# Performance work log

Hardware: AMD Instinct MI355X
Metric: run time of the kernel (lower is better)

The kernel has to match this reference:

```python
import jax, jax.numpy as jnp
import numpy as np

N = 100000   # nodes
E = 1600000  # edges
D = 128      # in = hid = out feature dim
EPS = 1e-5


def gcn_conv(x, W, b, src, dst, w, n):
    # PyG GCNConv: h = x W; symmetric normalization with self-loops already in (src,dst,w)
    h = x @ W                                        # [N, D]
    deg = jax.ops.segment_sum(w, dst, num_segments=n)
    dinv = jnp.where(deg > 0, deg ** -0.5, 0.0)
    norm = dinv[src] * w * dinv[dst]                 # [E+N]
    out = jax.ops.segment_sum(h[src] * norm[:, None], dst, num_segments=n)
    return out + b


def batch_norm(x, gamma, beta):
    m = x.mean(axis=0)
    v = x.var(axis=0)  # biased, as PyTorch uses for normalization
    return gamma * (x - m) * jax.lax.rsqrt(v + EPS) + beta


def setup_inputs() -> dict:
    key = jax.random.key(0)
    ks = jax.random.split(key, 10)
    x = jax.random.normal(ks[0], (N, D), dtype=jnp.float32)
    edge_index = jax.random.randint(ks[1], (2, E), 0, N, dtype=jnp.int64)
    edge_weight = jax.random.uniform(ks[2], (E,), dtype=jnp.float32)
    s = 1.0 / np.sqrt(D)
    W1 = jax.random.uniform(ks[3], (D, D), jnp.float32, -s, s)
    b1 = jax.random.uniform(ks[4], (D,), jnp.float32, -s, s)
    W2 = jax.random.uniform(ks[5], (D, D), jnp.float32, -s, s)
    b2 = jax.random.uniform(ks[6], (D,), jnp.float32, -s, s)
    g1 = jnp.ones((D,), jnp.float32); beta1 = jnp.zeros((D,), jnp.float32)
    g2 = jnp.ones((D,), jnp.float32); beta2 = jnp.zeros((D,), jnp.float32)
    return {"x": x, "edge_index": edge_index, "edge_weight": edge_weight,
            "W1": W1, "b1": b1, "W2": W2, "b2": b2,
            "g1": g1, "beta1": beta1, "g2": g2, "beta2": beta2}


def reference(x, edge_index, edge_weight, W1, b1, W2, b2, g1, beta1, g2, beta2):
    loops = jnp.arange(N, dtype=edge_index.dtype)
    src = jnp.concatenate([edge_index[0], loops])
    dst = jnp.concatenate([edge_index[1], loops])
    w = jnp.concatenate([edge_weight, jnp.ones((N,), edge_weight.dtype)])
    # layer 1: GCNConv -> BN -> relu (dropout inactive in eval)
    h = gcn_conv(x, W1, b1, src, dst, w, N)
    h = jax.nn.relu(batch_norm(h, g1, beta1))
    # layer 2
    h = gcn_conv(h, W2, b2, src, dst, w, N)
    h = jax.nn.relu(batch_norm(h, g2, beta2))
    return h
```

## Files before the change

kernel.cpp:

```cpp
#include <hip/hip_runtime.h>
#include <hip/hip_bf16.h>

#define NN 100000
#define EE 1600000
#define DD 128
#define CAP 56
#define NB 391
#define CAPB 6144
#define NRG 6250
#define NC 16
#define BN_EPS 1e-5f

typedef __attribute__((ext_vector_type(8))) short short8;
typedef __attribute__((ext_vector_type(4))) float f32x4;
typedef __attribute__((ext_vector_type(4))) unsigned int u32x4;

__device__ __forceinline__ float bfu2f(unsigned short u) {
    return __uint_as_float(((unsigned int)u) << 16);
}
__device__ __forceinline__ unsigned short f2bfu(float f) {
    unsigned int u = __float_as_uint(f);
    unsigned int r = (u + 0x7fffu + ((u >> 16) & 1u)) >> 16;
    return (unsigned short)r;
}
__device__ __forceinline__ void atomAddF(float* p, float v) {
    unsafeAtomicAdd(p, v);
}
__device__ __forceinline__ float ldF(const void* __restrict__ p, int isf32, size_t idx) {
    return isf32 ? ((const float*)p)[idx]
                 : bfu2f(((const unsigned short*)p)[idx]);
}
__device__ __forceinline__ int edge_at(const int* __restrict__ ei, int is64, unsigned int pos) {
    return is64 ? ei[(size_t)pos * 2] : ei[pos];
}

__global__ __launch_bounds__(256) void prep2(const int* __restrict__ ei,
                                             const unsigned int* __restrict__ g1w,
                                             const void* __restrict__ W1,
                                             const void* __restrict__ W2,
                                             int* __restrict__ flags,
                                             unsigned int* __restrict__ cursor,
                                             float* __restrict__ stats,
                                             unsigned short* __restrict__ Wt1,
                                             unsigned short* __restrict__ Wt2) {
    int t = threadIdx.x;
    int b = blockIdx.x;
    int isf32 = (g1w[0] == 0x3F800000u) ? 1 : 0;
    if (b == 0) {
        __shared__ int nz;
        if (t == 0) nz = 0;
        __syncthreads();
        if (ei[2 * t + 1] != 0) atomicExch(&nz, 1);
        __syncthreads();
        if (t == 0) {
            flags[0] = (nz == 0) ? 1 : 0;
            flags[1] = isf32;
        }
        stats[t] = 0.f;
        stats[512 + t] = 0.f;
    } else if (b == 129) {
        for (int i = t; i < 512; i += 256) cursor[i] = 0;
    } else {
        int i = (b - 1) * 256 + t;
        if (i < 16384) {
            int r = i >> 7, c = i & 127;
            Wt1[c * DD + r] = f2bfu(ldF(W1, isf32, i));
        } else {
            int j = i - 16384;
            int r = j >> 7, c = j & 127;
            Wt2[c * DD + r] = f2bfu(ldF(W2, isf32, j));
        }
    }
}

__device__ __forceinline__ void load_arow(const void* __restrict__ Xv, int isf32,
                                          int row, int quad, short8* dst) {
#pragma unroll
    for (int k4 = 0; k4 < 4; ++k4) {
        int k = k4 * 32 + quad * 8;
        if (isf32) {
            const float* xf = (const float*)Xv + (size_t)row * DD + k;
            float4 f0 = *(const float4*)xf;
            float4 f1 = *(const float4*)(xf + 4);
            short8 a;
            a[0] = (short)f2bfu(f0.x); a[1] = (short)f2bfu(f0.y);
            a[2] = (short)f2bfu(f0.z); a[3] = (short)f2bfu(f0.w);
            a[4] = (short)f2bfu(f1.x); a[5] = (short)f2bfu(f1.y);
            a[6] = (short)f2bfu(f1.z); a[7] = (short)f2bfu(f1.w);
            dst[k4] = a;
        } else {
            dst[k4] = *(const short8*)((const short*)Xv + (size_t)row * DD + k);
        }
    }
}

__global__ __launch_bounds__(256) void fatk(const void* __restrict__ Xv,
                                            const int* __restrict__ flags,
                                            const unsigned short* __restrict__ Wt,
                                            unsigned short* __restrict__ H,
                                            const int* __restrict__ ei,
                                            const void* __restrict__ w,
                                            uint2* __restrict__ staging,
                                            unsigned int* __restrict__ cursor) {
    unsigned int g = blockIdx.x;
    unsigned int q = g / 3u, r = g % 3u;
    if (r == 2u) {
        __shared__ unsigned int cnt[NB], base[NB];
        for (int i = threadIdx.x; i < NB; i += 256) cnt[i] = 0;
        __syncthreads();
        int is64 = flags[0], isf32 = flags[1];
        unsigned int e0 = q * 2048u;
        unsigned int lo[8], hi[8], rk[8];
        int bk[8];
#pragma unroll
        for (int i = 0; i < 8; ++i) {
            unsigned int e = e0 + i * 256u + threadIdx.x;
            bk[i] = -1;
            if (e < EE) {
                int s = edge_at(ei, is64, e);
                int d = edge_at(ei, is64, EE + e);
                float wv = ldF(w, isf32, e);
                unsigned int wfix = __float2uint_rn(wv * 16777216.0f);
                wfix = wfix > 0xFFFFFFu ? 0xFFFFFFu : wfix;
                lo[i] = ((unsigned int)f2bfu(wv) << 17) | (unsigned int)s;
                hi[i] = (wfix << 8) | (unsigned int)(d & 255);
                bk[i] = d >> 8;
                rk[i] = atomicAdd(&cnt[bk[i]], 1u);
            }
        }
        __syncthreads();
        for (int i = threadIdx.x; i < NB; i += 256)
            base[i] = cnt[i] ? atomicAdd(&cursor[i], cnt[i]) : 0u;
        __syncthreads();
#pragma unroll
        for (int i = 0; i < 8; ++i) {
            if (bk[i] >= 0) {
                unsigned int pos = base[bk[i]] + rk[i];
                if (pos < CAPB)
                    staging[(size_t)bk[i] * CAPB + pos] = make_uint2(lo[i], hi[i]);
            }
        }
    } else {
        int gid = (int)(q * 2u + r);
        int isf32 = flags[1];
        int lane = threadIdx.x & 63;
        int wave = threadIdx.x >> 6;
        int m = lane & 15, quad = lane >> 4;
        int n0 = wave * 32;
        const short* Ws = (const short*)Wt;
        short8 B0[4], B1[4];
#pragma unroll
        for (int k4 = 0; k4 < 4; ++k4) {
            int k = k4 * 32 + quad * 8;
            B0[k4] = *(const short8*)(Ws + (size_t)(n0 + m) * DD + k);
            B1[k4] = *(const short8*)(Ws + (size_t)(n0 + 16 + m) * DD + k);
        }
        int rgbase = gid * 4;
        short8 aC[4], aN[4];
        int rg0 = min(rgbase, NRG - 1);
        load_arow(Xv, isf32, rg0 * 16 + m, quad, aC);
#pragma unroll
        for (int rg = 0; rg < 4; ++rg) {
            int rgg = min(rgbase + rg, NRG - 1);
            if (rg < 3) {
                int rgn = min(rgbase + rg + 1, NRG - 1);
                load_arow(Xv, isf32, rgn * 16 + m, quad, aN);
            }
            f32x4 acc0 = {0.f, 0.f, 0.f, 0.f};
            f32x4 acc1 = {0.f, 0.f, 0.f, 0.f};
#pragma unroll
            for (int k4 = 0; k4 < 4; ++k4) {
                acc0 = __builtin_amdgcn_mfma_f32_16x16x32_bf16(aC[k4], B0[k4], acc0, 0, 0, 0);
                acc1 = __builtin_amdgcn_mfma_f32_16x16x32_bf16(aC[k4], B1[k4], acc1, 0, 0, 0);
            }
            int row0 = rgg * 16;
#pragma unroll
            for (int rr = 0; rr < 4; ++rr) {
                int crow = quad * 4 + rr;
                H[(size_t)(row0 + crow) * DD + n0 + m]      = f2bfu(acc0[rr]);
                H[(size_t)(row0 + crow) * DD + n0 + 16 + m] = f2bfu(acc1[rr]);
            }
#pragma unroll
            for (int k4 = 0; k4 < 4; ++k4) aC[k4] = aN[k4];
        }
    }
}

__global__ __launch_bounds__(256) void ellbuild(const uint2* __restrict__ staging,
                                                const unsigned int* __restrict__ cursor,
                                                unsigned int* __restrict__ ell,
                                                unsigned long long* __restrict__ meta,
                                                float* __restrict__ gacc) {
    __shared__ __align__(16) unsigned int lrow[256 * CAP];
    __shared__ unsigned int lcnt[256], lws[256];
    int b = blockIdx.x, t = threadIdx.x;
    if (b < 32) gacc[b * 256 + t] = 0.f;
    lcnt[t] = 0; lws[t] = 0;
    {
        uint4 z = make_uint4(0, 0, 0, 0);
        uint4* lp = (uint4*)lrow;
        for (int j = t; j < 256 * CAP / 4; j += 256) lp[j] = z;
    }
    __syncthreads();
    unsigned int rc = cursor[b];
    if (rc > CAPB) rc = CAPB;
    const uint2* S = staging + (size_t)b * CAPB;
    for (unsigned int j = t; j < rc; j += 256) {
        uint2 rec = S[j];
        unsigned int dl = rec.y & 255u;
        unsigned int rk = atomicAdd(&lcnt[dl], 1u);
        atomicAdd(&lws[dl], rec.y >> 8);
        if (rk < CAP) lrow[dl * CAP + rk] = rec.x;
    }
    __syncthreads();
    int nrows = NN - b * 256;
    if (nrows > 256) nrows = 256;
    int nv = nrows * (CAP / 4);
    uint4* dst = (uint4*)(ell + (size_t)b * 256 * CAP);
    const uint4* src = (const uint4*)lrow;
    for (int j = t; j < nv; j += 256) dst[j] = src[j];
    if (t < nrows) {
        unsigned int c = lcnt[t];
        unsigned int c8 = (c + 7u) & ~7u;
        if (c8 > CAP) c8 = CAP;
        float dv = rsqrtf(1.0f + (float)lws[t] * (1.0f / 16777216.0f));
        meta[b * 256 + t] = ((unsigned long long)c8 << 32) |
                            (unsigned long long)__float_as_uint(dv);
    }
}

__device__ __forceinline__ void proc4(u32x4 qv, const float* __restrict__ dvp,
                                      const unsigned short* __restrict__ Hf,
                                      float& a0, float& a1, float& a2, float& a3) {
    unsigned int qa[4] = {qv.x, qv.y, qv.z, qv.w};
#pragma unroll
    for (int t = 0; t < 4; ++t) {
        unsigned int ent = qa[t];
        int s = (int)(ent & 0x1FFFFu);
        float we = __uint_as_float((ent >> 1) & 0xFFFF0000u) * dvp[2 * s];
        ushort4 h = *(const ushort4*)(Hf + ((size_t)s << 7));
        a0 = fmaf(bfu2f(h.x), we, a0);
        a1 = fmaf(bfu2f(h.y), we, a1);
        a2 = fmaf(bfu2f(h.z), we, a2);
        a3 = fmaf(bfu2f(h.w), we, a3);
    }
}

__global__ __launch_bounds__(256) void gather_agg(const unsigned short* __restrict__ H,
                                                  const unsigned long long* __restrict__ meta,
                                                  const unsigned int* __restrict__ ell,
                                                  unsigned short* __restrict__ A,
                                                  float* __restrict__ gacc) {
    __shared__ float lsum[4][128], lss[4][128];
    int wave = threadIdx.x >> 6;
    int lane = threadIdx.x & 63;
    int half = lane >> 5;
    int sub = lane & 31;
    int n = blockIdx.x * 4 + wave;
    unsigned long long m = meta[n];
    int cnt8 = (int)(m >> 32);
    float di = __uint_as_float((unsigned int)m);
    const unsigned short* Hf = H + sub * 4;
    const float* dvp = (const float*)meta;
    float a0 = 0.f, a1 = 0.f, a2 = 0.f, a3 = 0.f;
    if (half == 0) {
        ushort4 hs = *(const ushort4*)(Hf + ((size_t)n << 7));
        a0 = bfu2f(hs.x) * di; a1 = bfu2f(hs.y) * di;
        a2 = bfu2f(hs.z) * di; a3 = bfu2f(hs.w) * di;
    }
    const unsigned int* row = ell + (size_t)n * CAP + (half << 2);
    if (cnt8 > 0) {
        u32x4 qc = __builtin_nontemporal_load((const u32x4*)row);
        u32x4 qn = __builtin_nontemporal_load((const u32x4*)(row + 8));
        for (int i = 0; i + 8 < cnt8; i += 8) {
            u32x4 qf = __builtin_nontemporal_load((const u32x4*)(row + i + 16));
            proc4(qc, dvp, Hf, a0, a1, a2, a3);
            qc = qn; qn = qf;
        }
        proc4(qc, dvp, Hf, a0, a1, a2, a3);
    }
    a0 += __shfl_down(a0, 32);
    a1 += __shfl_down(a1, 32);
    a2 += __shfl_down(a2, 32);
    a3 += __shfl_down(a3, 32);
    if (half == 0) {
        ushort4 o;
        o.x = f2bfu(a0 * di);
        o.y = f2bfu(a1 * di);
        o.z = f2bfu(a2 * di);
        o.w = f2bfu(a3 * di);
        *(ushort4*)(A + ((size_t)n << 7) + sub * 4) = o;
        float v0 = bfu2f(o.x), v1 = bfu2f(o.y), v2 = bfu2f(o.z), v3 = bfu2f(o.w);
        int fb = sub * 4;
        lsum[wave][fb + 0] = v0; lsum[wave][fb + 1] = v1;
        lsum[wave][fb + 2] = v2; lsum[wave][fb + 3] = v3;
        lss[wave][fb + 0] = v0 * v0; lss[wave][fb + 1] = v1 * v1;
        lss[wave][fb + 2] = v2 * v2; lss[wave][fb + 3] = v3 * v3;
    }
    __syncthreads();
    int t = threadIdx.x;
    if (t < 128) {
        float s = lsum[0][t] + lsum[1][t] + lsum[2][t] + lsum[3][t];
        float q = lss[0][t] + lss[1][t] + lss[2][t] + lss[3][t];
        float* gb = gacc + (blockIdx.x & (NC - 1)) * 256;
        atomAddF(&gb[t], s);
        atomAddF(&gb[128 + t], q);
    }
}

__global__ __launch_bounds__(256) void gemm2(const unsigned short* __restrict__ A,
                                             const float* __restrict__ scale,
                                             const float* __restrict__ shift,
                                             const unsigned short* __restrict__ Wt,
                                             unsigned short* __restrict__ H) {
    __shared__ __align__(16) float lsc[DD], lsh[DD];
    if (threadIdx.x < DD) {
        lsc[threadIdx.x] = scale[threadIdx.x];
        lsh[threadIdx.x] = shift[threadIdx.x];
    }
    __syncthreads();
    int lane = threadIdx.x & 63;
    int wave = threadIdx.x >> 6;
    int m = lane & 15, quad = lane >> 4;
    int n0 = wave * 32;
    const short* Ws = (const short*)Wt;
    short8 B0[4], B1[4];
#pragma unroll
    for (int k4 = 0; k4 < 4; ++k4) {
        int k = k4 * 32 + quad * 8;
        B0[k4] = *(const short8*)(Ws + (size_t)(n0 + m) * DD + k);
        B1[k4] = *(const short8*)(Ws + (size_t)(n0 + 16 + m) * DD + k);
    }
    int rgbase = blockIdx.x * 4;
    short8 aC[4], aN[4];
#define LOADA2(dst, RG)                                                           \
    {                                                                             \
        int rr_ = (RG) * 16 + m;                                                  \
        const short* ap_ = (const short*)A + (size_t)rr_ * DD;                    \
        _Pragma("unroll")                                                         \
        for (int k4_ = 0; k4_ < 4; ++k4_) {                                       \
            int k_ = k4_ * 32 + quad * 8;                                         \
            short8 raw_ = *(const short8*)(ap_ + k_);                             \
            float4 sc0_ = *(const float4*)(lsc + k_);                             \
            float4 sc1_ = *(const float4*)(lsc + k_ + 4);                         \
            float4 sh0_ = *(const float4*)(lsh + k_);                             \
            float4 sh1_ = *(const float4*)(lsh + k_ + 4);                         \
            short8 a_;                                                            \
            a_[0] = (short)f2bfu(fmaxf(fmaf(bfu2f((unsigned short)raw_[0]), sc0_.x, sh0_.x), 0.f)); \
            a_[1] = (short)f2bfu(fmaxf(fmaf(bfu2f((unsigned short)raw_[1]), sc0_.y, sh0_.y), 0.f)); \
            a_[2] = (short)f2bfu(fmaxf(fmaf(bfu2f((unsigned short)raw_[2]), sc0_.z, sh0_.z), 0.f)); \
            a_[3] = (short)f2bfu(fmaxf(fmaf(bfu2f((unsigned short)raw_[3]), sc0_.w, sh0_.w), 0.f)); \
            a_[4] = (short)f2bfu(fmaxf(fmaf(bfu2f((unsigned short)raw_[4]), sc1_.x, sh1_.x), 0.f)); \
            a_[5] = (short)f2bfu(fmaxf(fmaf(bfu2f((unsigned short)raw_[5]), sc1_.y, sh1_.y), 0.f)); \
            a_[6] = (short)f2bfu(fmaxf(fmaf(bfu2f((unsigned short)raw_[6]), sc1_.z, sh1_.z), 0.f)); \
            a_[7] = (short)f2bfu(fmaxf(fmaf(bfu2f((unsigned short)raw_[7]), sc1_.w, sh1_.w), 0.f)); \
            dst[k4_] = a_;                                                        \
        }                                                                         \
    }
    int rg0 = min(rgbase, NRG - 1);
    LOADA2(aC, rg0);
#pragma unroll
    for (int rg = 0; rg < 4; ++rg) {
        int rgg = min(rgbase + rg, NRG - 1);
        if (rg < 3) {
            int rgn = min(rgbase + rg + 1, NRG - 1);
            LOADA2(aN, rgn);
        }
        f32x4 acc0 = {0.f, 0.f, 0.f, 0.f};
        f32x4 acc1 = {0.f, 0.f, 0.f, 0.f};
#pragma unroll
        for (int k4 = 0; k4 < 4; ++k4) {
            acc0 = __builtin_amdgcn_mfma_f32_16x16x32_bf16(aC[k4], B0[k4], acc0, 0, 0, 0);
            acc1 = __builtin_amdgcn_mfma_f32_16x16x32_bf16(aC[k4], B1[k4], acc1, 0, 0, 0);
        }
        int row0 = rgg * 16;
#pragma unroll
        for (int rr = 0; rr < 4; ++rr) {
            int crow = quad * 4 + rr;
            H[(size_t)(row0 + crow) * DD + n0 + m]      = f2bfu(acc0[rr]);
            H[(size_t)(row0 + crow) * DD + n0 + 16 + m] = f2bfu(acc1[rr]);
        }
#pragma unroll
        for (int k4 = 0; k4 < 4; ++k4) aC[k4] = aN[k4];
    }
#undef LOADA2
}

__global__ __launch_bounds__(128) void bn_final(const float* __restrict__ gacc,
                                                const void* __restrict__ gamma,
                                                const void* __restrict__ beta,
                                                const int* __restrict__ flags,
                                                float* __restrict__ scale,
                                                float* __restrict__ shift) {
    int f = threadIdx.x;
    int isf32 = flags[1];
    float s = 0.f, ss = 0.f;
#pragma unroll
    for (int c = 0; c < NC; ++c) {
        s  += gacc[c * 256 + f];
        ss += gacc[c * 256 + 128 + f];
    }
    float m = s * (1.0f / NN);
    float v = ss * (1.0f / NN) - m * m;
    v = fmaxf(v, 0.0f);
    float sc = ldF(gamma, isf32, f) * rsqrtf(v + BN_EPS);
    scale[f] = sc;
    shift[f] = ldF(beta, isf32, f) - m * sc;
}

__global__ __launch_bounds__(256) void bn_apply(const unsigned short* __restrict__ A,
                                                const float* __restrict__ scale,
                                                const float* __restrict__ shift,
                                                const int* __restrict__ flags,
                                                void* __restrict__ out) {
    int i = blockIdx.x * 256 + threadIdx.x;
    int f = (i & 31) * 4;
    ushort4 v4 = ((const ushort4*)A)[i];
    float r0 = fmaxf(fmaf(bfu2f(v4.x), scale[f + 0], shift[f + 0]), 0.f);
    float r1 = fmaxf(fmaf(bfu2f(v4.y), scale[f + 1], shift[f + 1]), 0.f);
    float r2 = fmaxf(fmaf(bfu2f(v4.z), scale[f + 2], shift[f + 2]), 0.f);
    float r3 = fmaxf(fmaf(bfu2f(v4.w), scale[f + 3], shift[f + 3]), 0.f);
    if (flags[1]) {
        ((float4*)out)[i] = make_float4(r0, r1, r2, r3);
    } else {
        ushort4 o;
        o.x = f2bfu(r0); o.y = f2bfu(r1); o.z = f2bfu(r2); o.w = f2bfu(r3);
        ((ushort4*)out)[i] = o;
    }
}

extern "C" void kernel_launch(void* const* d_in, const int* in_sizes, int n_in,
                              void* d_out, int out_size, void* d_ws, size_t ws_size,
                              hipStream_t stream) {
    const void* x   = d_in[0];
    const int*  ei  = (const int*)d_in[1];
    const void* ew  = d_in[2];
    const void* W1  = d_in[3];
    const void* W2  = d_in[5];
    const void* g1  = d_in[7];
    const void* be1 = d_in[8];
    const void* g2  = d_in[9];
    const void* be2 = d_in[10];

    char* ws = (char*)d_ws;
    float* stats         = (float*)ws;
    int*   flags         = (int*)(ws + 4096);
    unsigned short* Wt1  = (unsigned short*)(ws + 4224);
    unsigned short* Wt2  = (unsigned short*)(ws + 36992);
    unsigned long long* meta = (unsigned long long*)(ws + 69760);
    unsigned int* ell    = (unsigned int*)(ws + 869760);
    unsigned short* Hbuf = (unsigned short*)(ws + 23269760);
    unsigned short* A    = (unsigned short*)(ws + 48869760);
    uint2* staging       = (uint2*)(ws + 48869760);
    unsigned int* cursor = (unsigned int*)(ws + 48869760 + 19218432);
    float* gaccL1 = (float*)(ws + 4224);
    float* gaccL2 = (float*)(ws + 4224 + 16384);
    float* scale1 = stats + 256, *shift1 = stats + 384;
    float* scale2 = stats + 768, *shift2 = stats + 896;

    prep2<<<130, 256, 0, stream>>>(ei, (const unsigned int*)g1, W1, W2,
                                   flags, cursor, stats, Wt1, Wt2);

    fatk<<<2346, 256, 0, stream>>>(x, flags, Wt1, Hbuf, ei, ew, staging, cursor);
    ellbuild<<<NB, 256, 0, stream>>>(staging, cursor, ell, meta, gaccL1);
    gather_agg<<<25000, 256, 0, stream>>>(Hbuf, meta, ell, A, gaccL1);
    bn_final<<<1, 128, 0, stream>>>(gaccL1, g1, be1, flags, scale1, shift1);

    gemm2<<<1563, 256, 0, stream>>>(A, scale1, shift1, Wt2, Hbuf);
    gather_agg<<<25000, 256, 0, stream>>>(Hbuf, meta, ell, A, gaccL2);
    bn_final<<<1, 128, 0, stream>>>(gaccL2, g2, be2, flags, scale2, shift2);
    bn_apply<<<12500, 256, 0, stream>>>(A, scale2, shift2, flags, d_out);
}
```

Baseline: 371.6 us.

## Stage GEMM outputs through LDS for 16-byte stores; process two nodes per wave in aggregation

Both MFMA GEMM epilogues now write the accumulators into a padded per-wave LDS tile and read them back row-contiguously. Each lane then emits one 16-byte bf16 store instead of eight scattered 2-byte stores. The gather-aggregation kernel now has each wave handle two nodes, accumulating the BN partial sums in registers, and launches half as many blocks. The aim is to cut store transactions and per-block reduction overhead, at the cost of extra LDS traffic and fewer resident waves. It relies on in-wave LDS write/read ordering without an explicit barrier.

```diff
diff --git a/kernel.cpp b/kernel.cpp
--- a/kernel.cpp
+++ b/kernel.cpp
@@ -102,6 +102,7 @@
                                             const void* __restrict__ w,
                                             uint2* __restrict__ staging,
                                             unsigned int* __restrict__ cursor) {
+    __shared__ __align__(16) float lc[4][16][36];
     unsigned int g = blockIdx.x;
     unsigned int q = g / 3u, r = g % 3u;
     if (r == 2u) {
@@ -146,6 +147,7 @@
         int lane = threadIdx.x & 63;
         int wave = threadIdx.x >> 6;
         int m = lane & 15, quad = lane >> 4;
+        int orow = lane >> 2, ocq = lane & 3;
         int n0 = wave * 32;
         const short* Ws = (const short*)Wt;
         short8 B0[4], B1[4];
@@ -173,13 +175,20 @@
                 acc0 = __builtin_amdgcn_mfma_f32_16x16x32_bf16(aC[k4], B0[k4], acc0, 0, 0, 0);
                 acc1 = __builtin_amdgcn_mfma_f32_16x16x32_bf16(aC[k4], B1[k4], acc1, 0, 0, 0);
             }
+#pragma unroll
+            for (int rr = 0; rr < 4; ++rr) {
+                lc[wave][quad * 4 + rr][m]      = acc0[rr];
+                lc[wave][quad * 4 + rr][16 + m] = acc1[rr];
+            }
+            float4 c0 = *(const float4*)&lc[wave][orow][ocq * 8];
+            float4 c1 = *(const float4*)&lc[wave][orow][ocq * 8 + 4];
+            short8 o;
+            o[0] = (short)f2bfu(c0.x); o[1] = (short)f2bfu(c0.y);
+            o[2] = (short)f2bfu(c0.z); o[3] = (short)f2bfu(c0.w);
+            o[4] = (short)f2bfu(c1.x); o[5] = (short)f2bfu(c1.y);
+            o[6] = (short)f2bfu(c1.z); o[7] = (short)f2bfu(c1.w);
             int row0 = rgg * 16;
-#pragma unroll
-            for (int rr = 0; rr < 4; ++rr) {
-                int crow = quad * 4 + rr;
-                H[(size_t)(row0 + crow) * DD + n0 + m]      = f2bfu(acc0[rr]);
-                H[(size_t)(row0 + crow) * DD + n0 + 16 + m] = f2bfu(acc1[rr]);
-            }
+            *(short8*)(H + (size_t)(row0 + orow) * DD + n0 + ocq * 8) = o;
 #pragma unroll
             for (int k4 = 0; k4 < 4; ++k4) aC[k4] = aN[k4];
         }
@@ -256,46 +265,55 @@
     int lane = threadIdx.x & 63;
     int half = lane >> 5;
     int sub = lane & 31;
-    int n = blockIdx.x * 4 + wave;
-    unsigned long long m = meta[n];
-    int cnt8 = (int)(m >> 32);
-    float di = __uint_as_float((unsigned int)m);
     const unsigned short* Hf = H + sub * 4;
     const float* dvp = (const float*)meta;
-    float a0 = 0.f, a1 = 0.f, a2 = 0.f, a3 = 0.f;
+    float sv0 = 0.f, sv1 = 0.f, sv2 = 0.f, sv3 = 0.f;
+    float sq0 = 0.f, sq1 = 0.f, sq2 = 0.f, sq3 = 0.f;
+#pragma unroll
+    for (int u = 0; u < 2; ++u) {
+        int n = blockIdx.x * 8 + wave * 2 + u;
+        unsigned long long m = meta[n];
+        int cnt8 = (int)(m >> 32);
+        float di = __uint_as_float((unsigned int)m);
+        float a0 = 0.f, a1 = 0.f, a2 = 0.f, a3 = 0.f;
+        if (half == 0) {
+            ushort4 hs = *(const ushort4*)(Hf + ((size_t)n << 7));
+            a0 = bfu2f(hs.x) * di; a1 = bfu2f(hs.y) * di;
+            a2 = bfu2f(hs.z) * di; a3 = bfu2f(hs.w) * di;
+        }
+        const unsigned int* row = ell + (size_t)n * CAP + (half << 2);
+        if (cnt8 > 0) {
+            u32x4 qc = __builtin_nontemporal_load((const u32x4*)row);
+            u32x4 qn = __builtin_nontemporal_load((const u32x4*)(row + 8));
+            for (int i = 0; i + 8 < cnt8; i += 8) {
+                u32x4 qf = __builtin_nontemporal_load((const u32x4*)(row + i + 16));
+                proc4(qc, dvp, Hf, a0, a1, a2, a3);
+                qc = qn; qn = qf;
+            }
+            proc4(qc, dvp, Hf, a0, a1, a2, a3);
+        }
+        a0 += __shfl_down(a0, 32);
+        a1 += __shfl_down(a1, 32);
+        a2 += __shfl_down(a2, 32);
+        a3 += __shfl_down(a3, 32);
+        if (half == 0) {
+            ushort4 o;
+            o.x = f2bfu(a0 * di);
+            o.y = f2bfu(a1 * di);
+            o.z = f2bfu(a2 * di);
+            o.w = f2bfu(a3 * di);
+            *(ushort4*)(A + ((size_t)n << 7) + sub * 4) = o;
+            float v0 = bfu2f(o.x), v1 = bfu2f(o.y), v2 = bfu2f(o.z), v3 = bfu2f(o.w);
+            sv0 += v0; sv1 += v1; sv2 += v2; sv3 += v3;
+            sq0 += v0 * v0; sq1 += v1 * v1; sq2 += v2 * v2; sq3 += v3 * v3;
+        }
+    }
     if (half == 0) {
-        ushort4 hs = *(const ushort4*)(Hf + ((size_t)n << 7));
-        a0 = bfu2f(hs.x) * di; a1 = bfu2f(hs.y) * di;
-        a2 = bfu2f(hs.z) * di; a3 = bfu2f(hs.w) * di;
-    }
-    const unsigned int* row = ell + (size_t)n * CAP + (half << 2);
-    if (cnt8 > 0) {
-        u32x4 qc = __builtin_nontemporal_load((const u32x4*)row);
-        u32x4 qn = __builtin_nontemporal_load((const u32x4*)(row + 8));
-        for (int i = 0; i + 8 < cnt8; i += 8) {
-            u32x4 qf = __builtin_nontemporal_load((const u32x4*)(row + i + 16));
-            proc4(qc, dvp, Hf, a0, a1, a2, a3);
-            qc = qn; qn = qf;
-        }
-        proc4(qc, dvp, Hf, a0, a1, a2, a3);
-    }
-    a0 += __shfl_down(a0, 32);
-    a1 += __shfl_down(a1, 32);
-    a2 += __shfl_down(a2, 32);
-    a3 += __shfl_down(a3, 32);
-    if (half == 0) {
-        ushort4 o;
-        o.x = f2bfu(a0 * di);
-        o.y = f2bfu(a1 * di);
-        o.z = f2bfu(a2 * di);
-        o.w = f2bfu(a3 * di);
-        *(ushort4*)(A + ((size_t)n << 7) + sub * 4) = o;
-        float v0 = bfu2f(o.x), v1 = bfu2f(o.y), v2 = bfu2f(o.z), v3 = bfu2f(o.w);
         int fb = sub * 4;
-        lsum[wave][fb + 0] = v0; lsum[wave][fb + 1] = v1;
-        lsum[wave][fb + 2] = v2; lsum[wave][fb + 3] = v3;
-        lss[wave][fb + 0] = v0 * v0; lss[wave][fb + 1] = v1 * v1;
-        lss[wave][fb + 2] = v2 * v2; lss[wave][fb + 3] = v3 * v3;
+        lsum[wave][fb + 0] = sv0; lsum[wave][fb + 1] = sv1;
+        lsum[wave][fb + 2] = sv2; lsum[wave][fb + 3] = sv3;
+        lss[wave][fb + 0] = sq0; lss[wave][fb + 1] = sq1;
+        lss[wave][fb + 2] = sq2; lss[wave][fb + 3] = sq3;
     }
     __syncthreads();
     int t = threadIdx.x;
@@ -314,6 +332,7 @@
                                              const unsigned short* __restrict__ Wt,
                                              unsigned short* __restrict__ H) {
     __shared__ __align__(16) float lsc[DD], lsh[DD];
+    __shared__ __align__(16) float lc[4][16][36];
     if (threadIdx.x < DD) {
         lsc[threadIdx.x] = scale[threadIdx.x];
         lsh[threadIdx.x] = shift[threadIdx.x];
@@ -322,6 +341,7 @@
     int lane = threadIdx.x & 63;
     int wave = threadIdx.x >> 6;
     int m = lane & 15, quad = lane >> 4;
+    int orow = lane >> 2, ocq = lane & 3;
     int n0 = wave * 32;
     const short* Ws = (const short*)Wt;
     short8 B0[4], B1[4];
@@ -373,13 +393,20 @@
             acc0 = __builtin_amdgcn_mfma_f32_16x16x32_bf16(aC[k4], B0[k4], acc0, 0, 0, 0);
             acc1 = __builtin_amdgcn_mfma_f32_16x16x32_bf16(aC[k4], B1[k4], acc1, 0, 0, 0);
         }
+#pragma unroll
+        for (int rr = 0; rr < 4; ++rr) {
+            lc[wave][quad * 4 + rr][m]      = acc0[rr];
+            lc[wave][quad * 4 + rr][16 + m] = acc1[rr];
+        }
+        float4 c0 = *(const float4*)&lc[wave][orow][ocq * 8];
+        float4 c1 = *(const float4*)&lc[wave][orow][ocq * 8 + 4];
+        short8 o;
+        o[0] = (short)f2bfu(c0.x); o[1] = (short)f2bfu(c0.y);
+        o[2] = (short)f2bfu(c0.z); o[3] = (short)f2bfu(c0.w);
+        o[4] = (short)f2bfu(c1.x); o[5] = (short)f2bfu(c1.y);
+        o[6] = (short)f2bfu(c1.z); o[7] = (short)f2bfu(c1.w);
         int row0 = rgg * 16;
-#pragma unroll
-        for (int rr = 0; rr < 4; ++rr) {
-            int crow = quad * 4 + rr;
-            H[(size_t)(row0 + crow) * DD + n0 + m]      = f2bfu(acc0[rr]);
-            H[(size_t)(row0 + crow) * DD + n0 + 16 + m] = f2bfu(acc1[rr]);
-        }
+        *(short8*)(H + (size_t)(row0 + orow) * DD + n0 + ocq * 8) = o;
 #pragma unroll
         for (int k4 = 0; k4 < 4; ++k4) aC[k4] = aN[k4];
     }
@@ -463,11 +490,11 @@
 
     fatk<<<2346, 256, 0, stream>>>(x, flags, Wt1, Hbuf, ei, ew, staging, cursor);
     ellbuild<<<NB, 256, 0, stream>>>(staging, cursor, ell, meta, gaccL1);
-    gather_agg<<<25000, 256, 0, stream>>>(Hbuf, meta, ell, A, gaccL1);
+    gather_agg<<<12500, 256, 0, stream>>>(Hbuf, meta, ell, A, gaccL1);
     bn_final<<<1, 128, 0, stream>>>(gaccL1, g1, be1, flags, scale1, shift1);
 
     gemm2<<<1563, 256, 0, stream>>>(A, scale1, shift1, Wt2, Hbuf);
-    gather_agg<<<25000, 256, 0, stream>>>(Hbuf, meta, ell, A, gaccL2);
+    gather_agg<<<12500, 256, 0, stream>>>(Hbuf, meta, ell, A, gaccL2);
     bn_final<<<1, 128, 0, stream>>>(gaccL2, g2, be2, flags, scale2, shift2);
     bn_apply<<<12500, 256, 0, stream>>>(A, scale2, shift2, flags, d_out);
 }
```

Measured after the change: 359.5 us. 1.03x faster.
